# Performance work log

Hardware: AMD Instinct MI355X
Metric: run time of the kernel (lower is better)

## Reference

```python
import jax, jax.numpy as jnp
import numpy as np

B = 64          # batch of trees
L = 10          # gated internal levels below the root
H = 256         # hidden_size
E = 256         # embed_size
V = 64          # embedding vocab (relation/role types)
TOTAL = 2 ** (L + 1) - 2   # heap layout: level i (1..L) has 2^i nodes at offset 2^i - 2


def setup_inputs() -> dict:
    key = jax.random.key(0)
    k = jax.random.split(key, 7)
    s = 0.05
    return {
        "node_ids": jax.random.randint(k[0], (B, TOTAL), 0, V, dtype=jnp.int32),
        "emb_table": jax.random.normal(k[1], (V, E), jnp.float32) * s,
        # W: x-projections, order (forget, input, output, update)
        "W": jax.random.normal(k[2], (4, E, H), jnp.float32) * s,
        "bW": jax.random.normal(k[3], (4, H), jnp.float32) * s,
        # U: hidden projections, [gate, child] with gate order
        # (forget_left, forget_right, input, output, update), child order (left, right)
        "U": jax.random.normal(k[4], (5, 2, H, H), jnp.float32) * s,
        "Ws": jax.random.normal(k[5], (2 * H, 3), jnp.float32) * s,
        "bs": jax.random.normal(k[6], (3,), jnp.float32) * s,
    }


def _tree_lstm(node_ids, emb_table, W, bW, U, Ws, bs):
    Bn, total = node_ids.shape
    Lv = int(np.log2(total + 2)) - 1          # number of gated levels (static)
    Hh = U.shape[-1]
    # Wforget is shared by both forget gates (as in the original module)
    gate_map = jnp.array([0, 0, 1, 2, 3])      # x-projection index per gate
    h = c = None
    for lev in range(Lv, 0, -1):               # leaves-up level order
        n = 2 ** lev
        off = 2 ** lev - 2
        ids = node_ids[:, off:off + n]         # [B, n]
        x = emb_table[ids]                     # [B, n, E]
        xg = jnp.einsum('bne,geh->gbnh', x, W) + bW[:, None, None, :]  # [4,B,n,H]
        if h is None:
            # deepest level: children are leaves -> zero h and c (init_hidden())
            hl = hr = cl = cr = jnp.zeros((Bn, n, Hh), x.dtype)
        else:
            hl, hr = h[:, 0::2], h[:, 1::2]
            cl, cr = c[:, 0::2], c[:, 1::2]
        pre = (jnp.einsum('bnh,ghk->gbnk', hl, U[:, 0])
               + jnp.einsum('bnh,ghk->gbnk', hr, U[:, 1])
               + xg[gate_map])                 # [5,B,n,H]
        f_l = jax.nn.sigmoid(pre[0])
        f_r = jax.nn.sigmoid(pre[1])
        i_g = jax.nn.sigmoid(pre[2])
        o_g = jax.nn.sigmoid(pre[3])
        u_g = jnp.tanh(pre[4])
        c = i_g * u_g + f_l * cl + f_r * cr
        h = o_g * jnp.tanh(c)
    # root: concatenate the two children's hidden states, then score
    root_hidden = jnp.concatenate([h[:, 0], h[:, 1]], axis=-1)   # [B, 2H]
    scores = root_hidden @ Ws + bs                               # [B, 3]
    return scores, root_hidden


def reference(node_ids, emb_table, W, bW, U, Ws, bs):
    return _tree_lstm(node_ids, emb_table, W, bW, U, Ws, bs)
```

## Files before the change

### kernel.cpp

```cpp
#include <hip/hip_runtime.h>
#include <hip/hip_bf16.h>
#include <stdint.h>
#include <math.h>


typedef __bf16 bf16x8 __attribute__((ext_vector_type(8)));
typedef float  f32x4  __attribute__((ext_vector_type(4)));
typedef int    i32x4  __attribute__((ext_vector_type(4)));

__device__ __forceinline__ float sigf(float x) { return 1.f / (1.f + __expf(-x)); }
__device__ __forceinline__ float tanhfast(float x) {
    return 1.f - 2.f / (__expf(2.f * x) + 1.f);
}

__global__ void xg_prep(const float* __restrict__ emb, const float* __restrict__ W,
                        const float* __restrict__ bW, float* __restrict__ xg4) {
    int g = blockIdx.x >> 6, v = blockIdx.x & 63, k = threadIdx.x;
    __shared__ float e[256];
    e[k] = emb[v * 256 + k];
    __syncthreads();
    float s = bW[g * 256 + k];
    const float* Wg = W + g * 65536 + k;
#pragma unroll 4
    for (int i = 0; i < 256; i++) s += e[i] * Wg[i * 256];
    xg4[(v * 256 + k) * 4 + g] = s;
}

__global__ void bt_prep(const float* __restrict__ U, __bf16* __restrict__ BtP) {
    int t = blockIdx.x * 256 + threadIdx.x;
    int g    = t >> 14;
    int r    = t & 16383;
    int ct   = r >> 10;
    int ks   = (r >> 6) & 15;
    int lane = t & 63;
    int lr = lane & 15, q = lane >> 4;
    int col = ct * 16 + lr;
    int kbase = ks * 32 + q * 8;
    bf16x8 v8;
#pragma unroll
    for (int e = 0; e < 8; e++) {
        int k = kbase + e;
        int s = k >> 8, kk = k & 255;
        v8[e] = (__bf16)U[((g * 2 + s) * 256 + kk) * 256 + col];
    }
    *(bf16x8*)(BtP + (long)t * 8) = v8;
}

__global__ void leaf_kernel(const int* __restrict__ ids, const float* __restrict__ xg4,
                            __bf16* __restrict__ h, __bf16* __restrict__ c) {
    int col = threadIdx.x;
    int r0 = blockIdx.x * 32;
    for (int r = r0; r < r0 + 32; r++) {
        int b = r >> 10, j = r & 1023;
        int id = ids[b * 2046 + 1022 + j];
        f32x4 xv = *(const f32x4*)(xg4 + (id * 256 + col) * 4);
        float ig = sigf(xv.y);
        float og = sigf(xv.z);
        float ug = tanhfast(xv.w);
        float cv = ig * ug;
        float hv = og * tanhfast(cv);
        h[r * 256 + col] = (__bf16)hv;
        c[r * 256 + col] = (__bf16)cv;
    }
}

__global__ __launch_bounds__(1024, 4) void level_kernel(
    const __bf16* __restrict__ A, const __bf16* __restrict__ Cprev,
    const __bf16* __restrict__ BtP, const float* __restrict__ xg4,
    const int* __restrict__ ids, __bf16* __restrict__ h_out,
    __bf16* __restrict__ c_out, float* __restrict__ rh_out,
    int lev, int M, int RG, int NB, int NB16) {
    __shared__ __bf16 Blds[5 * 16 * 512];
    const int gid = blockIdx.x;
    int rgslot, ct;
    if (NB16) { rgslot = gid & 15; ct = gid >> 4; }
    else      { rgslot = gid % NB; ct = gid / NB; }
    const int tid  = threadIdx.x;
    const int wave = tid >> 6;
    const int lane = tid & 63;
    const int lr = lane & 15, q = lane >> 4;
    const int gcol = ct * 16 + lr;
    const int n = 1 << lev;

#pragma unroll
    for (int i = 0; i < 5; i++) {
        int cc = tid + i * 1024;
        int g = cc >> 10;
        int r = cc & 1023;
        *(i32x4*)(&Blds[g * 8192 + r * 8]) =
            *(const i32x4*)(BtP + (long)(g * 16 + ct) * 8192 + r * 8);
    }
    __syncthreads();

    int rg0 = rgslot;
    long wrow = (long)rg0 * 512 + wave * 32;
    const __bf16* Ap = A + (wrow + lr) * 512 + q * 8;
    bf16x8 af[4][2];
    if (wrow < M) {
#pragma unroll
        for (int mt = 0; mt < 2; mt++) {
            af[0][mt] = *(const bf16x8*)(Ap + mt * 8192);
            af[1][mt] = *(const bf16x8*)(Ap + mt * 8192 + 32);
        }
    }

    for (int rg = rg0; rg < RG; rg += NB) {
        wrow = (long)rg * 512 + wave * 32;
        const bool active = (wrow < M);

        int rgn = rg + NB;
        long wrown = (rgn < RG) ? ((long)rgn * 512 + wave * 32) : wrow;
        const __bf16* Apn = A + (wrown + lr) * 512 + q * 8;

        int idv[2][4];
        __bf16 clv[2][4], crv[2][4];
        if (active) {
#pragma unroll
            for (int mt = 0; mt < 2; mt++)
#pragma unroll
                for (int v = 0; v < 4; v++) {
                    long grow = wrow + mt * 16 + q * 4 + v;
                    int b = (int)(grow >> lev);
                    int j = (int)(grow & (n - 1));
                    idv[mt][v] = ids[b * 2046 + (n - 2) + j];
                    clv[mt][v] = Cprev[grow * 512 + gcol];
                    crv[mt][v] = Cprev[grow * 512 + 256 + gcol];
                }
        }

        if (active) {
            f32x4 acc[5][2];
#pragma unroll
            for (int g2 = 0; g2 < 5; g2++)
#pragma unroll
                for (int mt = 0; mt < 2; mt++)
                    acc[g2][mt] = (f32x4){0.f, 0.f, 0.f, 0.f};

            bf16x8 bb[2][5];
#pragma unroll
            for (int g2 = 0; g2 < 5; g2++)
                bb[0][g2] = *(const bf16x8*)(&Blds[g2 * 8192 + lane * 8]);

#pragma unroll
            for (int s = 0; s < 16; s++) {
                {
                    int sp = s + 2;
                    const __bf16* P = (sp < 16) ? Ap : Apn;
                    int so = sp & 15;
#pragma unroll
                    for (int mt = 0; mt < 2; mt++)
                        af[sp & 3][mt] = *(const bf16x8*)(P + mt * 8192 + so * 32);
                }
                if (s + 1 < 16) {
#pragma unroll
                    for (int g2 = 0; g2 < 5; g2++)
                        bb[(s + 1) & 1][g2] =
                            *(const bf16x8*)(&Blds[g2 * 8192 + (s + 1) * 512 + lane * 8]);
                }
#pragma unroll
                for (int g2 = 0; g2 < 5; g2++)
#pragma unroll
                    for (int mt = 0; mt < 2; mt++)
                        acc[g2][mt] = __builtin_amdgcn_mfma_f32_16x16x32_bf16(
                            af[s & 3][mt], bb[s & 1][g2], acc[g2][mt], 0, 0, 0);
            }

#pragma unroll
            for (int mt = 0; mt < 2; mt++) {
#pragma unroll
                for (int v = 0; v < 4; v++) {
                    long grow = wrow + mt * 16 + q * 4 + v;
                    f32x4 xv = *(const f32x4*)(xg4 + (idv[mt][v] * 256 + gcol) * 4);
                    float fl = sigf(acc[0][mt][v] + xv.x);
                    float fr = sigf(acc[1][mt][v] + xv.x);
                    float ig = sigf(acc[2][mt][v] + xv.y);
                    float og = sigf(acc[3][mt][v] + xv.z);
                    float ug = tanhfast(acc[4][mt][v] + xv.w);
                    float cv = ig * ug + fl * (float)clv[mt][v]
                                       + fr * (float)crv[mt][v];
                    float hv = og * tanhfast(cv);
                    h_out[grow * 256 + gcol] = (__bf16)hv;
                    c_out[grow * 256 + gcol] = (__bf16)cv;
                    if (rh_out) rh_out[grow * 256 + gcol] = hv;
                }
            }
        }
        Ap = Apn;
    }
}

__global__ void scores_kernel(const float* __restrict__ rh, const float* __restrict__ Ws,
                              const float* __restrict__ bs, float* __restrict__ out) {
    int b = blockIdx.x;
    int t = threadIdx.x >> 6, lane = threadIdx.x & 63;
    float s = 0.f;
    for (int i = lane; i < 512; i += 64) s += rh[b * 512 + i] * Ws[i * 3 + t];
    for (int o = 32; o > 0; o >>= 1) s += __shfl_down(s, o);
    if (lane == 0) out[b * 3 + t] = s + bs[t];
}

extern "C" void kernel_launch(void* const* d_in, const int* in_sizes, int n_in,
                              void* d_out, int out_size, void* d_ws, size_t ws_size,
                              hipStream_t stream) {
    const int*   ids = (const int*)  d_in[0];
    const float* emb = (const float*)d_in[1];
    const float* W   = (const float*)d_in[2];
    const float* bW  = (const float*)d_in[3];
    const float* U   = (const float*)d_in[4];
    const float* Ws  = (const float*)d_in[5];
    const float* bs  = (const float*)d_in[6];
    float* out = (float*)d_out;

    char* ws = (char*)d_ws;
    float*  xg4 = (float*)ws;
    __bf16* BtP = (__bf16*)(ws + 262144);
    __bf16* h0  = (__bf16*)(ws + 1572864);
    __bf16* c0  = (__bf16*)(ws + 35127296);
    __bf16* h1  = (__bf16*)(ws + 68681728);
    __bf16* c1  = (__bf16*)(ws + 85458944);

    xg_prep<<<dim3(256), dim3(256), 0, stream>>>(emb, W, bW, xg4);
    bt_prep<<<dim3(320), dim3(256), 0, stream>>>(U, BtP);
    leaf_kernel<<<dim3(2048), dim3(256), 0, stream>>>(ids, xg4, h0, c0);

    __bf16* hb[2] = {h0, h1};
    __bf16* cb[2] = {c0, c1};
    int cur = 0;
    for (int lev = 9; lev >= 1; lev--) {
        int M = 64 << lev;
        int RG = M >> 9; if (RG < 1) RG = 1;
        int NB = (RG < 16) ? RG : 16;
        float* rh = (lev == 1) ? (out + 192) : nullptr;
        level_kernel<<<dim3(16 * NB), dim3(1024), 0, stream>>>(
            hb[cur], cb[cur], BtP, xg4, ids, hb[1 - cur], cb[1 - cur], rh,
            lev, M, RG, NB, (NB == 16) ? 1 : 0);
        cur = 1 - cur;
    }
    scores_kernel<<<dim3(64), dim3(192), 0, stream>>>(out + 192, Ws, bs, out);
}
```

Measured before the change: 415.7 us.

## Fuse top tree levels into per-tree LDS-resident subtree kernel with scores

```diff
diff --git a/kernel.cpp b/kernel.cpp
--- a/kernel.cpp
+++ b/kernel.cpp
@@ -13,37 +13,38 @@
     return 1.f - 2.f / (__expf(2.f * x) + 1.f);
 }
 
-__global__ void xg_prep(const float* __restrict__ emb, const float* __restrict__ W,
-                        const float* __restrict__ bW, float* __restrict__ xg4) {
-    int g = blockIdx.x >> 6, v = blockIdx.x & 63, k = threadIdx.x;
-    __shared__ float e[256];
-    e[k] = emb[v * 256 + k];
-    __syncthreads();
-    float s = bW[g * 256 + k];
-    const float* Wg = W + g * 65536 + k;
+__global__ void prep_kernel(const float* __restrict__ emb, const float* __restrict__ W,
+                            const float* __restrict__ bW, const float* __restrict__ U,
+                            float* __restrict__ xg4, __bf16* __restrict__ BtP) {
+    if (blockIdx.x < 256) {
+        int g = blockIdx.x >> 6, v = blockIdx.x & 63, k = threadIdx.x;
+        __shared__ float e[256];
+        e[k] = emb[v * 256 + k];
+        __syncthreads();
+        float s = bW[g * 256 + k];
+        const float* Wg = W + g * 65536 + k;
 #pragma unroll 4
-    for (int i = 0; i < 256; i++) s += e[i] * Wg[i * 256];
-    xg4[(v * 256 + k) * 4 + g] = s;
-}
-
-__global__ void bt_prep(const float* __restrict__ U, __bf16* __restrict__ BtP) {
-    int t = blockIdx.x * 256 + threadIdx.x;
-    int g    = t >> 14;
-    int r    = t & 16383;
-    int ct   = r >> 10;
-    int ks   = (r >> 6) & 15;
-    int lane = t & 63;
-    int lr = lane & 15, q = lane >> 4;
-    int col = ct * 16 + lr;
-    int kbase = ks * 32 + q * 8;
-    bf16x8 v8;
-#pragma unroll
-    for (int e = 0; e < 8; e++) {
-        int k = kbase + e;
-        int s = k >> 8, kk = k & 255;
-        v8[e] = (__bf16)U[((g * 2 + s) * 256 + kk) * 256 + col];
-    }
-    *(bf16x8*)(BtP + (long)t * 8) = v8;
+        for (int i = 0; i < 256; i++) s += e[i] * Wg[i * 256];
+        xg4[(v * 256 + k) * 4 + g] = s;
+    } else {
+        int t = (blockIdx.x - 256) * 256 + threadIdx.x;
+        int g    = t >> 14;
+        int r    = t & 16383;
+        int ct   = r >> 10;
+        int ks   = (r >> 6) & 15;
+        int lane = t & 63;
+        int lr = lane & 15, q = lane >> 4;
+        int col = ct * 16 + lr;
+        int kbase = ks * 32 + q * 8;
+        bf16x8 v8;
+#pragma unroll
+        for (int e2 = 0; e2 < 8; e2++) {
+            int k = kbase + e2;
+            int s = k >> 8, kk = k & 255;
+            v8[e2] = (__bf16)U[((g * 2 + s) * 256 + kk) * 256 + col];
+        }
+        *(bf16x8*)(BtP + (long)t * 8) = v8;
+    }
 }
 
 __global__ void leaf_kernel(const int* __restrict__ ids, const float* __restrict__ xg4,
@@ -189,14 +190,130 @@
     }
 }
 
-__global__ void scores_kernel(const float* __restrict__ rh, const float* __restrict__ Ws,
-                              const float* __restrict__ bs, float* __restrict__ out) {
-    int b = blockIdx.x;
-    int t = threadIdx.x >> 6, lane = threadIdx.x & 63;
-    float s = 0.f;
-    for (int i = lane; i < 512; i += 64) s += rh[b * 512 + i] * Ws[i * 3 + t];
-    for (int o = 32; o > 0; o >>= 1) s += __shfl_down(s, o);
-    if (lane == 0) out[b * 3 + t] = s + bs[t];
+__global__ __launch_bounds__(1024, 4) void subtree_kernel(
+    const __bf16* __restrict__ Hin, const __bf16* __restrict__ Cin,
+    const __bf16* __restrict__ BtP, const float* __restrict__ xg4,
+    const int* __restrict__ ids, const float* __restrict__ Ws,
+    const float* __restrict__ bs, float* __restrict__ out) {
+    __shared__ __bf16 hbuf[128 * 256];
+    __shared__ __bf16 cbuf[128 * 256];
+    __shared__ float  rhl[512];
+    const int b    = blockIdx.x;
+    const int tid  = threadIdx.x;
+    const int wave = tid >> 6;
+    const int lane = tid & 63;
+    const int lr = lane & 15, q = lane >> 4;
+    const int ct = wave;
+    const int gcol = ct * 16 + lr;
+
+#pragma unroll
+    for (int i = 0; i < 4; i++) {
+        int idx = tid + i * 1024;
+        int row = idx >> 5;
+        int colb = (idx & 31) * 16;
+        int dst = (row * 512 + colb) ^ (((row >> 1) & 7) << 4);
+        *(i32x4*)((char*)hbuf + dst) =
+            *(const i32x4*)(Hin + (long)(b * 128 + row) * 256 + (idx & 31) * 8);
+        *(i32x4*)((char*)cbuf + dst) =
+            *(const i32x4*)(Cin + (long)(b * 128 + row) * 256 + (idx & 31) * 8);
+    }
+    __syncthreads();
+
+    for (int lev = 6; lev >= 1; lev--) {
+        const int n   = 1 << lev;
+        const int off = n - 2;
+        const int nch = (n > 32) ? 2 : 1;
+        for (int ch = 0; ch < nch; ch++) {
+            const int rbase = ch * 32;
+            int idv[2][4];
+            float clv[2][4], crv[2][4];
+#pragma unroll
+            for (int mt = 0; mt < 2; mt++)
+#pragma unroll
+                for (int v = 0; v < 4; v++) {
+                    int j = rbase + mt * 16 + q * 4 + v;
+                    idv[mt][v] = ids[b * 2046 + off + j];
+                    int c0r = 2 * j, c1r = 2 * j + 1;
+                    int a0 = (c0r * 512 + gcol * 2) ^ (((c0r >> 1) & 7) << 4);
+                    int a1 = (c1r * 512 + gcol * 2) ^ (((c1r >> 1) & 7) << 4);
+                    clv[mt][v] = (float)*(const __bf16*)((const char*)cbuf + a0);
+                    crv[mt][v] = (float)*(const __bf16*)((const char*)cbuf + a1);
+                }
+
+            f32x4 acc[5][2];
+#pragma unroll
+            for (int g2 = 0; g2 < 5; g2++)
+#pragma unroll
+                for (int mt = 0; mt < 2; mt++)
+                    acc[g2][mt] = (f32x4){0.f, 0.f, 0.f, 0.f};
+
+            const __bf16* Bp = BtP + (long)ct * 8192;
+            bf16x8 bb[2][5];
+#pragma unroll
+            for (int g2 = 0; g2 < 5; g2++)
+                bb[0][g2] = *(const bf16x8*)(Bp + (long)g2 * 131072 + lane * 8);
+
+#pragma unroll
+            for (int s = 0; s < 16; s++) {
+                if (s + 1 < 16) {
+#pragma unroll
+                    for (int g2 = 0; g2 < 5; g2++)
+                        bb[(s + 1) & 1][g2] = *(const bf16x8*)(
+                            Bp + (long)g2 * 131072 + (s + 1) * 512 + lane * 8);
+                }
+                bf16x8 af[2];
+#pragma unroll
+                for (int mt = 0; mt < 2; mt++) {
+                    int j0 = rbase + mt * 16 + lr;
+                    int crow = 2 * j0 + (s >> 3);
+                    int ab = (crow * 512 + ((s & 7) * 64 + q * 16))
+                             ^ (((crow >> 1) & 7) << 4);
+                    af[mt] = *(const bf16x8*)((const char*)hbuf + ab);
+                }
+#pragma unroll
+                for (int g2 = 0; g2 < 5; g2++)
+#pragma unroll
+                    for (int mt = 0; mt < 2; mt++)
+                        acc[g2][mt] = __builtin_amdgcn_mfma_f32_16x16x32_bf16(
+                            af[mt], bb[s & 1][g2], acc[g2][mt], 0, 0, 0);
+            }
+            __syncthreads();
+
+#pragma unroll
+            for (int mt = 0; mt < 2; mt++) {
+#pragma unroll
+                for (int v = 0; v < 4; v++) {
+                    int j = rbase + mt * 16 + q * 4 + v;
+                    if (j < n) {
+                        f32x4 xv = *(const f32x4*)(xg4 + (idv[mt][v] * 256 + gcol) * 4);
+                        float fl = sigf(acc[0][mt][v] + xv.x);
+                        float fr = sigf(acc[1][mt][v] + xv.x);
+                        float ig = sigf(acc[2][mt][v] + xv.y);
+                        float og = sigf(acc[3][mt][v] + xv.z);
+                        float ug = tanhfast(acc[4][mt][v] + xv.w);
+                        float cv = ig * ug + fl * clv[mt][v] + fr * crv[mt][v];
+                        float hv = og * tanhfast(cv);
+                        int dst = (j * 512 + gcol * 2) ^ (((j >> 1) & 7) << 4);
+                        *(__bf16*)((char*)hbuf + dst) = (__bf16)hv;
+                        if (lev > 1) *(__bf16*)((char*)cbuf + dst) = (__bf16)cv;
+                        if (lev == 1) {
+                            out[192 + b * 512 + j * 256 + gcol] = hv;
+                            rhl[j * 256 + gcol] = hv;
+                        }
+                    }
+                }
+            }
+            __syncthreads();
+        }
+    }
+
+    if (tid < 192) {
+        int t = tid >> 6, ln = tid & 63;
+        float s = 0.f;
+        for (int i = ln; i < 512; i += 64) s += rhl[i] * Ws[i * 3 + t];
+        for (int o = 32; o > 0; o >>= 1) s += __shfl_down(s, o);
+        if (ln == 0) out[b * 3 + t] = s + bs[t];
+    }
 }
 
 extern "C" void kernel_launch(void* const* d_in, const int* in_sizes, int n_in,
@@ -219,22 +336,21 @@
     __bf16* h1  = (__bf16*)(ws + 68681728);
     __bf16* c1  = (__bf16*)(ws + 85458944);
 
-    xg_prep<<<dim3(256), dim3(256), 0, stream>>>(emb, W, bW, xg4);
-    bt_prep<<<dim3(320), dim3(256), 0, stream>>>(U, BtP);
+    prep_kernel<<<dim3(576), dim3(256), 0, stream>>>(emb, W, bW, U, xg4, BtP);
     leaf_kernel<<<dim3(2048), dim3(256), 0, stream>>>(ids, xg4, h0, c0);
 
     __bf16* hb[2] = {h0, h1};
     __bf16* cb[2] = {c0, c1};
     int cur = 0;
-    for (int lev = 9; lev >= 1; lev--) {
+    for (int lev = 9; lev >= 7; lev--) {
         int M = 64 << lev;
-        int RG = M >> 9; if (RG < 1) RG = 1;
+        int RG = M >> 9;
         int NB = (RG < 16) ? RG : 16;
-        float* rh = (lev == 1) ? (out + 192) : nullptr;
         level_kernel<<<dim3(16 * NB), dim3(1024), 0, stream>>>(
-            hb[cur], cb[cur], BtP, xg4, ids, hb[1 - cur], cb[1 - cur], rh,
+            hb[cur], cb[cur], BtP, xg4, ids, hb[1 - cur], cb[1 - cur], nullptr,
             lev, M, RG, NB, (NB == 16) ? 1 : 0);
         cur = 1 - cur;
     }
-    scores_kernel<<<dim3(64), dim3(192), 0, stream>>>(out + 192, Ws, bs, out);
-}
+    subtree_kernel<<<dim3(64), dim3(1024), 0, stream>>>(
+        h1, c1, BtP, xg4, ids, Ws, bs, out);
+}
```

New measurement: 584.9 us. 40.7% more time.
